# Kernel optimization log

Hardware: AMD Instinct MI355X
Metric: run time of the kernel (lower is better)

Reference implementation:

```python
import jax, jax.numpy as jnp
import numpy as np

# Geometry constants from init_kwargs
GRID = (128, 128, 128)
SIZE = np.array([2.0, 2.0, 2.0], dtype=np.float32)
CENTER = np.array([0.0, 0.0, 0.0], dtype=np.float32)
ORIGIN = CENTER - SIZE / 2.0                      # lower corner of the voxel box
VOXEL = SIZE / np.array(GRID, dtype=np.float32)   # voxel pitch per axis
N_LORS = 100000


def siddon_project(image, lors):
    """Exact Siddon line-integral forward projection, fully vectorized.

    image: [Gx,Gy,Gz] voxel values; lors: [N,6] = (x0,y0,z0, x1,y1,z1).
    For each ray we compute all intersection parameters alpha with the
    grid planes, sort them, and accumulate segment_length * voxel_value.
    """
    gx, gy, gz = GRID
    origin = jnp.asarray(ORIGIN)
    voxel = jnp.asarray(VOXEL)
    grid_f = jnp.asarray(np.array(GRID, dtype=np.float32))

    p0 = lors[:, 0:3]                 # [N,3] ray start
    d = lors[:, 3:6] - p0             # [N,3] ray direction (p1 - p0)
    eps = jnp.float32(1e-9)
    d_safe = jnp.where(jnp.abs(d) < eps, eps, d)  # avoid div-by-zero; huge alphas get clipped away

    # Entry/exit parameters of the ray with the bounding box, clamped to the segment [0,1].
    bmin = origin
    bmax = origin + voxel * grid_f
    a0 = (bmin - p0) / d_safe         # [N,3]
    a1 = (bmax - p0) / d_safe
    amin = jnp.maximum(jnp.max(jnp.minimum(a0, a1), axis=1), 0.0)  # [N]
    amax = jnp.minimum(jnp.min(jnp.maximum(a0, a1), axis=1), 1.0)  # [N]

    def plane_alphas(axis, g):
        # alpha at every grid plane along `axis`: [N, g+1]
        planes = origin[axis] + jnp.arange(g + 1, dtype=jnp.float32) * voxel[axis]
        return (planes[None, :] - p0[:, axis:axis + 1]) / d_safe[:, axis:axis + 1]

    # All candidate alphas, clipped into [amin, amax] then merge-sorted per ray.
    alphas = jnp.concatenate(
        [plane_alphas(0, gx), plane_alphas(1, gy), plane_alphas(2, gz),
         amin[:, None], amax[:, None]], axis=1)                      # [N, K+1]
    alphas = jnp.clip(alphas, amin[:, None], amax[:, None])
    alphas = jnp.sort(alphas, axis=1)

    diff = alphas[:, 1:] - alphas[:, :-1]                            # [N, K]
    ray_len = jnp.linalg.norm(d, axis=1, keepdims=True)              # [N, 1]
    seg = diff * ray_len                                             # intersection lengths

    # Voxel index from each segment midpoint.
    mid = alphas[:, :-1] + 0.5 * diff                                # [N, K]
    pts = p0[:, None, :] + mid[..., None] * d[:, None, :]            # [N, K, 3]
    idxf = jnp.floor((pts - origin) / voxel)                         # [N, K, 3]

    valid = (seg > 0) \
        & jnp.all((idxf >= 0) & (idxf < grid_f), axis=-1) \
        & (amax > amin)[:, None]
    idx = jnp.clip(idxf, 0.0, grid_f - 1.0).astype(jnp.int32)
    flat = (idx[..., 0] * gy + idx[..., 1]) * gz + idx[..., 2]       # [N, K]
    vals = jnp.take(image.reshape(-1), flat)
    return jnp.sum(jnp.where(valid, seg * vals, 0.0), axis=1)        # [N]


def setup_inputs() -> dict:
    key = jax.random.key(0)
    k1, k2 = jax.random.split(key)
    image = jax.random.uniform(k1, GRID, dtype=jnp.float32)          # nonneg activity volume
    lors = jax.random.normal(k2, (N_LORS, 6), dtype=jnp.float32)     # endpoints straddle [-1,1]^3 box
    return {"image": image, "lors": lors}


def reference(image, lors):
    return siddon_project(image, lors)
```

## Files before the change

kernel.cpp:

```cpp
#include <hip/hip_runtime.h>
#include <hip/hip_fp16.h>
#include <math.h>


static constexpr float VOX = 0.015625f;
static constexpr float INV_VOX = 64.0f;
static constexpr int   K = 16;
static constexpr int   LOGK = 4;
static constexpr int   NVOX = 128 * 128 * 128;
static constexpr int   IDX_MASK = 0x3FFFFE;

struct TState {
  float alx, aly, alz;
  float dax, day, daz;
  float acur, aend;
  int   ix, iy, iz;
  int   stx, sty, stz;
};

__device__ __forceinline__ int brick_addr(int ix, int iy, int iz) {
  int hx = ((ix & 0x7C) << 14) | ((ix & 3) << 4);
  int hy = ((iy & 0x7C) << 9)  | ((iy & 3) << 2);
  int hz = ((iz & 0x7C) << 4)  | (iz & 3);
  return ((hx | hy | hz) << 1) & IDX_MASK;
}

__device__ __forceinline__ void step4(const __half* __restrict__ image,
                                      TState& S, float dif4[4], float v4[4]) {
#pragma unroll
  for (int j = 0; j < 4; ++j) {
    float anext = fminf(fminf(S.alx, S.aly), S.alz);
    float astop = fminf(anext, S.aend);
    float dif   = fmaxf(astop - S.acur, 0.0f);
    dif4[j] = dif;
    int addr = (dif > 0.0f) ? brick_addr(S.ix, S.iy, S.iz) : 0;
    v4[j] = __half2float(*(const __half*)((const char*)image + addr));
    S.acur = astop;
    bool cx = S.alx <= anext;
    bool cy = S.aly <= anext;
    bool cz = S.alz <= anext;
    S.ix += cx ? S.stx : 0;  S.alx += cx ? S.dax : 0.0f;
    S.iy += cy ? S.sty : 0;  S.aly += cy ? S.day : 0.0f;
    S.iz += cz ? S.stz : 0;  S.alz += cz ? S.daz : 0.0f;
  }
}

__device__ __forceinline__ void axis_init(float astart, float aend, float p0,
                                          float ds, float inv,
                                          int& st, int& iv, float& al, float& da,
                                          int& cnt) {
  float ts = (fmaf(astart, ds, p0) + 1.0f) * INV_VOX;
  float te = (fmaf(aend,   ds, p0) + 1.0f) * INV_VOX;
  int ip;
  if (ds > 0.0f) {
    ip = (int)floorf(ts) + 1;
    int il = (int)floorf(te); if (il > 128) il = 128;
    cnt = il - ip + 1; st = 1; iv = ip - 1;
  } else {
    ip = (int)ceilf(ts) - 1;
    int il = (int)ceilf(te); if (il < 0) il = 0;
    cnt = ip - il + 1; st = -1; iv = ip;
  }
  if (cnt < 0) cnt = 0;
  al = (fmaf((float)ip, VOX, -1.0f) - p0) * inv;
  da = VOX * fabsf(inv);
}

__device__ __forceinline__ void ray_setup(const float* L,
    float& p0x, float& p0y, float& p0z,
    float& dx, float& dy, float& dz,
    float& dsx, float& dsy, float& dsz,
    float& invx, float& invy, float& invz,
    float& amin, float& amax) {
  p0x = L[0]; p0y = L[1]; p0z = L[2];
  dx = L[3] - p0x; dy = L[4] - p0y; dz = L[5] - p0z;
  const float eps = 1e-9f;
  dsx = (fabsf(dx) < eps) ? eps : dx;
  dsy = (fabsf(dy) < eps) ? eps : dy;
  dsz = (fabsf(dz) < eps) ? eps : dz;
  invx = __builtin_amdgcn_rcpf(dsx);
  invy = __builtin_amdgcn_rcpf(dsy);
  invz = __builtin_amdgcn_rcpf(dsz);
  float a0 = (-1.0f - p0x) * invx, a1 = (1.0f - p0x) * invx;
  float axmin = fminf(a0, a1), axmax = fmaxf(a0, a1);
  a0 = (-1.0f - p0y) * invy; a1 = (1.0f - p0y) * invy;
  float aymin = fminf(a0, a1), aymax = fmaxf(a0, a1);
  a0 = (-1.0f - p0z) * invz; a1 = (1.0f - p0z) * invz;
  float azmin = fminf(a0, a1), azmax = fmaxf(a0, a1);
  amin = fmaxf(fmaxf(axmin, aymin), fmaxf(azmin, 0.0f));
  amax = fminf(fminf(axmax, aymax), fminf(azmax, 1.0f));
}

__global__ __launch_bounds__(256) void convert_brick(
    const float* __restrict__ img, __half* __restrict__ h)
{
  int i = blockIdx.x * blockDim.x + threadIdx.x;
  int stride = gridDim.x * blockDim.x;
  for (int hi = i; hi < NVOX; hi += stride) {
    int lz = hi & 3, ly = (hi >> 2) & 3, lx = (hi >> 4) & 3;
    int bz = (hi >> 6) & 31, by = (hi >> 11) & 31, bx = (hi >> 16) & 31;
    int ix = (bx << 2) | lx, iy = (by << 2) | ly, iz = (bz << 2) | lz;
    h[hi] = __float2half(img[(((ix << 7) | iy) << 7) | iz]);
  }
}

__global__ __launch_bounds__(256) void siddon_fp(
    const __half* __restrict__ image,
    const float* __restrict__ lors,
    float* __restrict__ out, int n)
{
  int t   = blockIdx.x * blockDim.x + threadIdx.x;
  int ray = t >> LOGK;
  int k   = t & (K - 1);
  if (ray >= n) return;

  float p0x,p0y,p0z,dx,dy,dz,dsx,dsy,dsz,invx,invy,invz,amin,amax;
  ray_setup(lors + (long)ray * 6, p0x,p0y,p0z, dx,dy,dz,
            dsx,dsy,dsz, invx,invy,invz, amin,amax);

  float acc0 = 0.0f, acc1 = 0.0f;
  if (amax > amin) {
    float s      = (amax - amin) * (1.0f / (float)K);
    float astart = fmaf((float)k, s, amin);
    float aend   = (k == K - 1) ? amax : fmaf((float)(k + 1), s, amin);

    TState S;
    S.acur = astart; S.aend = aend;
    int c0, c1, c2;
    axis_init(astart, aend, p0x, dsx, invx, S.stx, S.ix, S.alx, S.dax, c0);
    axis_init(astart, aend, p0y, dsy, invy, S.sty, S.iy, S.aly, S.day, c1);
    axis_init(astart, aend, p0z, dsz, invz, S.stz, S.iz, S.alz, S.daz, c2);

    int ns = c0 + c1 + c2 + 2;
    int nb = (ns + 3) >> 2;
    if (nb < 2) nb = 2;

    float difA[4], difB[4], difC[4];
    float vA[4], vB[4], vC[4];

#define ISSUE(X)   step4(image, S, dif##X, v##X)
#define CONSUME(X)                                                  \
    do { acc0 = fmaf(dif##X[0], v##X[0], acc0);                     \
         acc1 = fmaf(dif##X[1], v##X[1], acc1);                     \
         acc0 = fmaf(dif##X[2], v##X[2], acc0);                     \
         acc1 = fmaf(dif##X[3], v##X[3], acc1); } while (0)

    ISSUE(A);
    ISSUE(B);
    int produce = nb - 2;
    while (produce >= 3) {
      ISSUE(C); CONSUME(A);
      ISSUE(A); CONSUME(B);
      ISSUE(B); CONSUME(C);
      produce -= 3;
    }
    if (produce == 2) {
      ISSUE(C); CONSUME(A);
      ISSUE(A); CONSUME(B);
      CONSUME(C); CONSUME(A);
    } else if (produce == 1) {
      ISSUE(C); CONSUME(A);
      CONSUME(B); CONSUME(C);
    } else {
      CONSUME(A); CONSUME(B);
    }
#undef ISSUE
#undef CONSUME

    float rlen = sqrtf(dx * dx + dy * dy + dz * dz);
    acc0 = (acc0 + acc1) * rlen;
    acc1 = 0.0f;
  }

  float acc = acc0 + acc1;
  acc += __shfl_xor(acc, 1);
  acc += __shfl_xor(acc, 2);
  acc += __shfl_xor(acc, 4);
  acc += __shfl_xor(acc, 8);
  if (k == 0) out[ray] = acc;
}

extern "C" void kernel_launch(void* const* d_in, const int* in_sizes, int n_in,
                              void* d_out, int out_size, void* d_ws, size_t ws_size,
                              hipStream_t stream) {
  const float* image = (const float*)d_in[0];
  const float* lors  = (const float*)d_in[1];
  float* out = (float*)d_out;
  int n = out_size;

  __half* h = (__half*)d_ws;
  hipLaunchKernelGGL(convert_brick, dim3(2048), dim3(256), 0, stream, image, h);

  long total = (long)n * K;
  int block = 256;
  int grid = (int)((total + block - 1) / block);
  hipLaunchKernelGGL(siddon_fp, dim3(grid), dim3(block), 0, stream,
                     h, lors, out, n);
}
```

Measured before the change: 54.57 us.

## Load-balance ray segments across block lanes proportional to voxel count

Each block now handles 16 rays. A setup phase counts the voxel crossings of every ray, and lanes are handed out to rays in proportion to that count from a budget of 240 lanes, replacing the fixed 16 lanes per ray. The per-lane traversal steps 2 voxels per batch instead of 4, which suits the shorter per-lane segments. The aim is to cut divergence and idle lanes caused by rays of very different lengths. In exchange it adds three block barriers, serial prefix work in one thread and a shared-memory reduction.

```diff
diff --git a/kernel.cpp b/kernel.cpp
--- a/kernel.cpp
+++ b/kernel.cpp
@@ -5,10 +5,11 @@
 
 static constexpr float VOX = 0.015625f;
 static constexpr float INV_VOX = 64.0f;
-static constexpr int   K = 16;
-static constexpr int   LOGK = 4;
 static constexpr int   NVOX = 128 * 128 * 128;
 static constexpr int   IDX_MASK = 0x3FFFFE;
+static constexpr int   RPB = 16;
+static constexpr int   TPB = 256;
+static constexpr int   BUDGET_LANES = 240;
 
 struct TState {
   float alx, aly, alz;
@@ -25,16 +26,16 @@
   return ((hx | hy | hz) << 1) & IDX_MASK;
 }
 
-__device__ __forceinline__ void step4(const __half* __restrict__ image,
-                                      TState& S, float dif4[4], float v4[4]) {
+__device__ __forceinline__ void step2(const __half* __restrict__ image,
+                                      TState& S, float dif2[2], float v2[2]) {
 #pragma unroll
-  for (int j = 0; j < 4; ++j) {
+  for (int j = 0; j < 2; ++j) {
     float anext = fminf(fminf(S.alx, S.aly), S.alz);
     float astop = fminf(anext, S.aend);
     float dif   = fmaxf(astop - S.acur, 0.0f);
-    dif4[j] = dif;
+    dif2[j] = dif;
     int addr = (dif > 0.0f) ? brick_addr(S.ix, S.iy, S.iz) : 0;
-    v4[j] = __half2float(*(const __half*)((const char*)image + addr));
+    v2[j] = __half2float(*(const __half*)((const char*)image + addr));
     S.acur = astop;
     bool cx = S.alx <= anext;
     bool cy = S.aly <= anext;
@@ -66,31 +67,6 @@
   da = VOX * fabsf(inv);
 }
 
-__device__ __forceinline__ void ray_setup(const float* L,
-    float& p0x, float& p0y, float& p0z,
-    float& dx, float& dy, float& dz,
-    float& dsx, float& dsy, float& dsz,
-    float& invx, float& invy, float& invz,
-    float& amin, float& amax) {
-  p0x = L[0]; p0y = L[1]; p0z = L[2];
-  dx = L[3] - p0x; dy = L[4] - p0y; dz = L[5] - p0z;
-  const float eps = 1e-9f;
-  dsx = (fabsf(dx) < eps) ? eps : dx;
-  dsy = (fabsf(dy) < eps) ? eps : dy;
-  dsz = (fabsf(dz) < eps) ? eps : dz;
-  invx = __builtin_amdgcn_rcpf(dsx);
-  invy = __builtin_amdgcn_rcpf(dsy);
-  invz = __builtin_amdgcn_rcpf(dsz);
-  float a0 = (-1.0f - p0x) * invx, a1 = (1.0f - p0x) * invx;
-  float axmin = fminf(a0, a1), axmax = fmaxf(a0, a1);
-  a0 = (-1.0f - p0y) * invy; a1 = (1.0f - p0y) * invy;
-  float aymin = fminf(a0, a1), aymax = fmaxf(a0, a1);
-  a0 = (-1.0f - p0z) * invz; a1 = (1.0f - p0z) * invz;
-  float azmin = fminf(a0, a1), azmax = fmaxf(a0, a1);
-  amin = fmaxf(fmaxf(axmin, aymin), fmaxf(azmin, 0.0f));
-  amax = fminf(fminf(axmax, aymax), fminf(azmax, 1.0f));
-}
-
 __global__ __launch_bounds__(256) void convert_brick(
     const float* __restrict__ img, __half* __restrict__ h)
 {
@@ -109,75 +85,159 @@
     const float* __restrict__ lors,
     float* __restrict__ out, int n)
 {
-  int t   = blockIdx.x * blockDim.x + threadIdx.x;
-  int ray = t >> LOGK;
-  int k   = t & (K - 1);
-  if (ray >= n) return;
-
-  float p0x,p0y,p0z,dx,dy,dz,dsx,dsy,dsz,invx,invy,invz,amin,amax;
-  ray_setup(lors + (long)ray * 6, p0x,p0y,p0z, dx,dy,dz,
-            dsx,dsy,dsz, invx,invy,invz, amin,amax);
+  __shared__ float sP[RPB][9];
+  __shared__ float sAmax[RPB], sRlen[RPB];
+  __shared__ int   sL[RPB];
+  __shared__ int   sLpref[RPB + 1];
+  __shared__ unsigned char sMap[TPB];
+  __shared__ float sPart[TPB];
+
+  const int tid = threadIdx.x;
+  const int rayBase = blockIdx.x * RPB;
+  const float eps = 1e-9f;
+
+  if (tid < RPB) {
+    int ray = rayBase + tid;
+    int Vp1 = 0;
+    float p0x = 0, p0y = 0, p0z = 0, dx = 0, dy = 0, dz = 0;
+    float amin = 0, amax = 0, rlen = 0;
+    if (ray < n) {
+      const float* L = lors + (long)ray * 6;
+      p0x = L[0]; p0y = L[1]; p0z = L[2];
+      dx = L[3] - p0x; dy = L[4] - p0y; dz = L[5] - p0z;
+      float dsx = (fabsf(dx) < eps) ? eps : dx;
+      float dsy = (fabsf(dy) < eps) ? eps : dy;
+      float dsz = (fabsf(dz) < eps) ? eps : dz;
+      float invx = __builtin_amdgcn_rcpf(dsx);
+      float invy = __builtin_amdgcn_rcpf(dsy);
+      float invz = __builtin_amdgcn_rcpf(dsz);
+      float a0 = (-1.0f - p0x) * invx, a1 = (1.0f - p0x) * invx;
+      float axmin = fminf(a0, a1), axmax = fmaxf(a0, a1);
+      a0 = (-1.0f - p0y) * invy; a1 = (1.0f - p0y) * invy;
+      float aymin = fminf(a0, a1), aymax = fmaxf(a0, a1);
+      a0 = (-1.0f - p0z) * invz; a1 = (1.0f - p0z) * invz;
+      float azmin = fminf(a0, a1), azmax = fmaxf(a0, a1);
+      amin = fmaxf(fmaxf(axmin, aymin), fmaxf(azmin, 0.0f));
+      amax = fminf(fminf(axmax, aymax), fminf(azmax, 1.0f));
+      if (amax > amin) {
+        int st, iv, c0, c1, c2; float al, da;
+        axis_init(amin, amax, p0x, dsx, invx, st, iv, al, da, c0);
+        axis_init(amin, amax, p0y, dsy, invy, st, iv, al, da, c1);
+        axis_init(amin, amax, p0z, dsz, invz, st, iv, al, da, c2);
+        Vp1 = c0 + c1 + c2 + 1;
+      }
+      rlen = sqrtf(dx * dx + dy * dy + dz * dz);
+    }
+    sL[tid] = Vp1;
+    sP[tid][0] = p0x; sP[tid][1] = p0y; sP[tid][2] = p0z;
+    sP[tid][3] = dx;  sP[tid][4] = dy;  sP[tid][5] = dz;
+    sP[tid][6] = amin;
+    sAmax[tid] = amax; sRlen[tid] = rlen;
+  }
+  sMap[tid] = 0xFF;
+  __syncthreads();
+
+  if (tid == 0) {
+    int T = 0;
+#pragma unroll
+    for (int r = 0; r < RPB; ++r) T += (sL[r] > 0) ? (sL[r] - 1) : 0;
+    int B = (T + BUDGET_LANES - 1) / BUDGET_LANES; if (B < 1) B = 1;
+    int acc = 0;
+#pragma unroll
+    for (int r = 0; r < RPB; ++r) {
+      sLpref[r] = acc;
+      int L = 0;
+      if (sL[r] > 0) { int V = sL[r] - 1; L = (V + B - 1) / B; if (L < 1) L = 1; }
+      sL[r] = L;
+      acc += L;
+    }
+    sLpref[RPB] = acc;
+  }
+  __syncthreads();
+
+  if (tid < RPB) {
+    int L = sL[tid];
+    if (L > 0)
+      sP[tid][7] = (sAmax[tid] - sP[tid][6]) * __builtin_amdgcn_rcpf((float)L);
+    int a = sLpref[tid], b = sLpref[tid + 1];
+    for (int j = a; j < b; ++j) sMap[j] = (unsigned char)tid;
+  }
+  __syncthreads();
 
   float acc0 = 0.0f, acc1 = 0.0f;
-  if (amax > amin) {
-    float s      = (amax - amin) * (1.0f / (float)K);
-    float astart = fmaf((float)k, s, amin);
-    float aend   = (k == K - 1) ? amax : fmaf((float)(k + 1), s, amin);
-
-    TState S;
-    S.acur = astart; S.aend = aend;
-    int c0, c1, c2;
-    axis_init(astart, aend, p0x, dsx, invx, S.stx, S.ix, S.alx, S.dax, c0);
-    axis_init(astart, aend, p0y, dsy, invy, S.sty, S.iy, S.aly, S.day, c1);
-    axis_init(astart, aend, p0z, dsz, invz, S.stz, S.iz, S.alz, S.daz, c2);
-
-    int ns = c0 + c1 + c2 + 2;
-    int nb = (ns + 3) >> 2;
-    if (nb < 2) nb = 2;
-
-    float difA[4], difB[4], difC[4];
-    float vA[4], vB[4], vC[4];
-
-#define ISSUE(X)   step4(image, S, dif##X, v##X)
+  int r = sMap[tid];
+  if (r != 0xFF) {
+    float p0x = sP[r][0], p0y = sP[r][1], p0z = sP[r][2];
+    float dx  = sP[r][3], dy  = sP[r][4], dz  = sP[r][5];
+    float amin = sP[r][6], s = sP[r][7], amax = sAmax[r];
+    int L = sL[r];
+    int c = tid - sLpref[r];
+
+    float astart = fmaf((float)c, s, amin);
+    float aend   = (c == L - 1) ? amax : fmaf((float)(c + 1), s, amin);
+
+    if (aend > astart) {
+      float dsx = (fabsf(dx) < eps) ? eps : dx;
+      float dsy = (fabsf(dy) < eps) ? eps : dy;
+      float dsz = (fabsf(dz) < eps) ? eps : dz;
+      float invx = __builtin_amdgcn_rcpf(dsx);
+      float invy = __builtin_amdgcn_rcpf(dsy);
+      float invz = __builtin_amdgcn_rcpf(dsz);
+
+      TState S;
+      S.acur = astart; S.aend = aend;
+      int c0, c1, c2;
+      axis_init(astart, aend, p0x, dsx, invx, S.stx, S.ix, S.alx, S.dax, c0);
+      axis_init(astart, aend, p0y, dsy, invy, S.sty, S.iy, S.aly, S.day, c1);
+      axis_init(astart, aend, p0z, dsz, invz, S.stz, S.iz, S.alz, S.daz, c2);
+
+      int ns = c0 + c1 + c2 + 2;
+      int nb = (ns + 1) >> 1;
+      if (nb < 2) nb = 2;
+
+      float difA[2], difB[2], difC[2];
+      float vA[2], vB[2], vC[2];
+
+#define ISSUE(X)   step2(image, S, dif##X, v##X)
 #define CONSUME(X)                                                  \
-    do { acc0 = fmaf(dif##X[0], v##X[0], acc0);                     \
-         acc1 = fmaf(dif##X[1], v##X[1], acc1);                     \
-         acc0 = fmaf(dif##X[2], v##X[2], acc0);                     \
-         acc1 = fmaf(dif##X[3], v##X[3], acc1); } while (0)
-
-    ISSUE(A);
-    ISSUE(B);
-    int produce = nb - 2;
-    while (produce >= 3) {
-      ISSUE(C); CONSUME(A);
-      ISSUE(A); CONSUME(B);
-      ISSUE(B); CONSUME(C);
-      produce -= 3;
-    }
-    if (produce == 2) {
-      ISSUE(C); CONSUME(A);
-      ISSUE(A); CONSUME(B);
-      CONSUME(C); CONSUME(A);
-    } else if (produce == 1) {
-      ISSUE(C); CONSUME(A);
-      CONSUME(B); CONSUME(C);
-    } else {
-      CONSUME(A); CONSUME(B);
-    }
+      do { acc0 = fmaf(dif##X[0], v##X[0], acc0);                   \
+           acc1 = fmaf(dif##X[1], v##X[1], acc1); } while (0)
+
+      ISSUE(A);
+      ISSUE(B);
+      int produce = nb - 2;
+      while (produce >= 3) {
+        ISSUE(C); CONSUME(A);
+        ISSUE(A); CONSUME(B);
+        ISSUE(B); CONSUME(C);
+        produce -= 3;
+      }
+      if (produce == 2) {
+        ISSUE(C); CONSUME(A);
+        ISSUE(A); CONSUME(B);
+        CONSUME(C); CONSUME(A);
+      } else if (produce == 1) {
+        ISSUE(C); CONSUME(A);
+        CONSUME(B); CONSUME(C);
+      } else {
+        CONSUME(A); CONSUME(B);
+      }
 #undef ISSUE
 #undef CONSUME
-
-    float rlen = sqrtf(dx * dx + dy * dy + dz * dz);
-    acc0 = (acc0 + acc1) * rlen;
-    acc1 = 0.0f;
-  }
-
-  float acc = acc0 + acc1;
-  acc += __shfl_xor(acc, 1);
-  acc += __shfl_xor(acc, 2);
-  acc += __shfl_xor(acc, 4);
-  acc += __shfl_xor(acc, 8);
-  if (k == 0) out[ray] = acc;
+    }
+  }
+  sPart[tid] = acc0 + acc1;
+  __syncthreads();
+
+  if (tid < RPB) {
+    int ray = rayBase + tid;
+    if (ray < n) {
+      float sum = 0.0f;
+      int a = sLpref[tid], b = sLpref[tid + 1];
+      for (int j = a; j < b; ++j) sum += sPart[j];
+      out[ray] = sum * sRlen[tid];
+    }
+  }
 }
 
 extern "C" void kernel_launch(void* const* d_in, const int* in_sizes, int n_in,
@@ -191,9 +251,7 @@
   __half* h = (__half*)d_ws;
   hipLaunchKernelGGL(convert_brick, dim3(2048), dim3(256), 0, stream, image, h);
 
-  long total = (long)n * K;
-  int block = 256;
-  int grid = (int)((total + block - 1) / block);
-  hipLaunchKernelGGL(siddon_fp, dim3(grid), dim3(block), 0, stream,
+  int grid = (n + RPB - 1) / RPB;
+  hipLaunchKernelGGL(siddon_fp, dim3(grid), dim3(256), 0, stream,
                      h, lors, out, n);
 }
```

Measured after the change: 60.57 us. +11.0%, slower.

## Sort rays by voxel count within each block and shrink step batch to 2

Applied to the files above, without the earlier changes.

Each block of 16 rays first computes every ray's total voxel-crossing count, ranks the rays by that count in shared memory, and assigns rays to 16-lane groups in sorted order. Rays of similar length then share a wavefront, which reduces divergence in the traversal loop. The per-thread step batch also drops from 4 to 2 steps, cutting wasted trailing steps but giving less prefetch depth. The cost is a redundant ray setup pass, two block-wide barriers, and rays being set up twice.

```diff
diff --git a/kernel.cpp b/kernel.cpp
--- a/kernel.cpp
+++ b/kernel.cpp
@@ -6,9 +6,9 @@
 static constexpr float VOX = 0.015625f;
 static constexpr float INV_VOX = 64.0f;
 static constexpr int   K = 16;
-static constexpr int   LOGK = 4;
 static constexpr int   NVOX = 128 * 128 * 128;
 static constexpr int   IDX_MASK = 0x3FFFFE;
+static constexpr int   RPB = 16;
 
 struct TState {
   float alx, aly, alz;
@@ -25,16 +25,16 @@
   return ((hx | hy | hz) << 1) & IDX_MASK;
 }
 
-__device__ __forceinline__ void step4(const __half* __restrict__ image,
-                                      TState& S, float dif4[4], float v4[4]) {
+__device__ __forceinline__ void step2(const __half* __restrict__ image,
+                                      TState& S, float dif2[2], float v2[2]) {
 #pragma unroll
-  for (int j = 0; j < 4; ++j) {
+  for (int j = 0; j < 2; ++j) {
     float anext = fminf(fminf(S.alx, S.aly), S.alz);
     float astop = fminf(anext, S.aend);
     float dif   = fmaxf(astop - S.acur, 0.0f);
-    dif4[j] = dif;
+    dif2[j] = dif;
     int addr = (dif > 0.0f) ? brick_addr(S.ix, S.iy, S.iz) : 0;
-    v4[j] = __half2float(*(const __half*)((const char*)image + addr));
+    v2[j] = __half2float(*(const __half*)((const char*)image + addr));
     S.acur = astop;
     bool cx = S.alx <= anext;
     bool cy = S.aly <= anext;
@@ -109,67 +109,103 @@
     const float* __restrict__ lors,
     float* __restrict__ out, int n)
 {
-  int t   = blockIdx.x * blockDim.x + threadIdx.x;
-  int ray = t >> LOGK;
-  int k   = t & (K - 1);
-  if (ray >= n) return;
-
-  float p0x,p0y,p0z,dx,dy,dz,dsx,dsy,dsz,invx,invy,invz,amin,amax;
-  ray_setup(lors + (long)ray * 6, p0x,p0y,p0z, dx,dy,dz,
-            dsx,dsy,dsz, invx,invy,invz, amin,amax);
+  __shared__ int sV[RPB];
+  __shared__ unsigned char sOrd[RPB];
+
+  const int tid = threadIdx.x;
+  const int rayBase = blockIdx.x * RPB;
+
+  if (tid < RPB) {
+    int ray = rayBase + tid;
+    int V = 0;
+    if (ray < n) {
+      float p0x,p0y,p0z,dx,dy,dz,dsx,dsy,dsz,invx,invy,invz,amin,amax;
+      ray_setup(lors + (long)ray * 6, p0x,p0y,p0z, dx,dy,dz,
+                dsx,dsy,dsz, invx,invy,invz, amin,amax);
+      if (amax > amin) {
+        int st, iv, c0, c1, c2; float al, da;
+        axis_init(amin, amax, p0x, dsx, invx, st, iv, al, da, c0);
+        axis_init(amin, amax, p0y, dsy, invy, st, iv, al, da, c1);
+        axis_init(amin, amax, p0z, dsz, invz, st, iv, al, da, c2);
+        V = c0 + c1 + c2 + 1;
+      }
+    }
+    sV[tid] = V;
+  }
+  __syncthreads();
+
+  if (tid < RPB) {
+    int v = sV[tid];
+    int rank = 0;
+#pragma unroll
+    for (int j = 0; j < RPB; ++j) {
+      int vj = sV[j];
+      rank += (vj > v) || (vj == v && j < tid);
+    }
+    sOrd[rank] = (unsigned char)tid;
+  }
+  __syncthreads();
+
+  int ray = rayBase + (int)sOrd[tid >> 4];
+  int k   = tid & (K - 1);
+  bool live = ray < n;
 
   float acc0 = 0.0f, acc1 = 0.0f;
-  if (amax > amin) {
-    float s      = (amax - amin) * (1.0f / (float)K);
-    float astart = fmaf((float)k, s, amin);
-    float aend   = (k == K - 1) ? amax : fmaf((float)(k + 1), s, amin);
-
-    TState S;
-    S.acur = astart; S.aend = aend;
-    int c0, c1, c2;
-    axis_init(astart, aend, p0x, dsx, invx, S.stx, S.ix, S.alx, S.dax, c0);
-    axis_init(astart, aend, p0y, dsy, invy, S.sty, S.iy, S.aly, S.day, c1);
-    axis_init(astart, aend, p0z, dsz, invz, S.stz, S.iz, S.alz, S.daz, c2);
-
-    int ns = c0 + c1 + c2 + 2;
-    int nb = (ns + 3) >> 2;
-    if (nb < 2) nb = 2;
-
-    float difA[4], difB[4], difC[4];
-    float vA[4], vB[4], vC[4];
-
-#define ISSUE(X)   step4(image, S, dif##X, v##X)
+  if (live) {
+    float p0x,p0y,p0z,dx,dy,dz,dsx,dsy,dsz,invx,invy,invz,amin,amax;
+    ray_setup(lors + (long)ray * 6, p0x,p0y,p0z, dx,dy,dz,
+              dsx,dsy,dsz, invx,invy,invz, amin,amax);
+
+    if (amax > amin) {
+      float s      = (amax - amin) * (1.0f / (float)K);
+      float astart = fmaf((float)k, s, amin);
+      float aend   = (k == K - 1) ? amax : fmaf((float)(k + 1), s, amin);
+
+      TState S;
+      S.acur = astart; S.aend = aend;
+      int c0, c1, c2;
+      axis_init(astart, aend, p0x, dsx, invx, S.stx, S.ix, S.alx, S.dax, c0);
+      axis_init(astart, aend, p0y, dsy, invy, S.sty, S.iy, S.aly, S.day, c1);
+      axis_init(astart, aend, p0z, dsz, invz, S.stz, S.iz, S.alz, S.daz, c2);
+
+      int ns = c0 + c1 + c2 + 2;
+      int nb = (ns + 1) >> 1;
+      if (nb < 2) nb = 2;
+
+      float difA[2], difB[2], difC[2];
+      float vA[2], vB[2], vC[2];
+
+#define ISSUE(X)   step2(image, S, dif##X, v##X)
 #define CONSUME(X)                                                  \
-    do { acc0 = fmaf(dif##X[0], v##X[0], acc0);                     \
-         acc1 = fmaf(dif##X[1], v##X[1], acc1);                     \
-         acc0 = fmaf(dif##X[2], v##X[2], acc0);                     \
-         acc1 = fmaf(dif##X[3], v##X[3], acc1); } while (0)
-
-    ISSUE(A);
-    ISSUE(B);
-    int produce = nb - 2;
-    while (produce >= 3) {
-      ISSUE(C); CONSUME(A);
-      ISSUE(A); CONSUME(B);
-      ISSUE(B); CONSUME(C);
-      produce -= 3;
-    }
-    if (produce == 2) {
-      ISSUE(C); CONSUME(A);
-      ISSUE(A); CONSUME(B);
-      CONSUME(C); CONSUME(A);
-    } else if (produce == 1) {
-      ISSUE(C); CONSUME(A);
-      CONSUME(B); CONSUME(C);
-    } else {
-      CONSUME(A); CONSUME(B);
-    }
+      do { acc0 = fmaf(dif##X[0], v##X[0], acc0);                   \
+           acc1 = fmaf(dif##X[1], v##X[1], acc1); } while (0)
+
+      ISSUE(A);
+      ISSUE(B);
+      int produce = nb - 2;
+      while (produce >= 3) {
+        ISSUE(C); CONSUME(A);
+        ISSUE(A); CONSUME(B);
+        ISSUE(B); CONSUME(C);
+        produce -= 3;
+      }
+      if (produce == 2) {
+        ISSUE(C); CONSUME(A);
+        ISSUE(A); CONSUME(B);
+        CONSUME(C); CONSUME(A);
+      } else if (produce == 1) {
+        ISSUE(C); CONSUME(A);
+        CONSUME(B); CONSUME(C);
+      } else {
+        CONSUME(A); CONSUME(B);
+      }
 #undef ISSUE
 #undef CONSUME
 
-    float rlen = sqrtf(dx * dx + dy * dy + dz * dz);
-    acc0 = (acc0 + acc1) * rlen;
-    acc1 = 0.0f;
+      float rlen = sqrtf(dx * dx + dy * dy + dz * dz);
+      acc0 = (acc0 + acc1) * rlen;
+      acc1 = 0.0f;
+    }
   }
 
   float acc = acc0 + acc1;
@@ -177,7 +213,7 @@
   acc += __shfl_xor(acc, 2);
   acc += __shfl_xor(acc, 4);
   acc += __shfl_xor(acc, 8);
-  if (k == 0) out[ray] = acc;
+  if (live && k == 0) out[ray] = acc;
 }
 
 extern "C" void kernel_launch(void* const* d_in, const int* in_sizes, int n_in,
@@ -191,9 +227,7 @@
   __half* h = (__half*)d_ws;
   hipLaunchKernelGGL(convert_brick, dim3(2048), dim3(256), 0, stream, image, h);
 
-  long total = (long)n * K;
-  int block = 256;
-  int grid = (int)((total + block - 1) / block);
-  hipLaunchKernelGGL(siddon_fp, dim3(grid), dim3(block), 0, stream,
+  int grid = (n + RPB - 1) / RPB;
+  hipLaunchKernelGGL(siddon_fp, dim3(grid), dim3(256), 0, stream,
                      h, lors, out, n);
 }
```

Result: faster. 53.38 us (-2.2%).
